# Optimization experiments

Hardware: AMD Instinct MI355X
Metric: run time of the kernel (lower is better)

The kernel has to match this reference:

```python
import jax, jax.numpy as jnp
import numpy as np

N, E, DN, DE, H, L = 2048, 32768, 512, 512, 8, 2
BN_EPS = 1e-5  # torch BatchNorm1d eps; eval mode with running_mean=0, running_var=1


def setup_inputs():
    key = jax.random.key(0)
    ks = jax.random.split(key, 12)
    rng = np.random.default_rng(0)
    # unique directed edges: 3E/4 upper-triangular pairs + reverses of the first E/4
    iu, ju = np.triu_indices(N, k=1)
    sel = rng.choice(iu.size, size=3 * E // 4, replace=False)
    s, d = iu[sel], ju[sel]
    src = np.concatenate([s, d[: E // 4]])
    dst = np.concatenate([d, s[: E // 4]])
    edge_index = jnp.asarray(np.stack([src, dst]).astype(np.int32))

    def p(k, shape, fan_in):
        return jax.random.normal(k, shape, jnp.float32) / np.sqrt(fan_in).astype(np.float32)

    return dict(
        x=jax.random.normal(ks[0], (N, DN), jnp.float32),
        edge_feature=jax.random.normal(ks[1], (E, DE), jnp.float32),
        node_pos=jax.random.uniform(ks[2], (N, 3), jnp.float32) * 10.0,
        inw=p(ks[3], (L, 3 * DN, DN), DN),          # MHA in_proj_weight per layer
        inb=jnp.zeros((L, 3 * DN), jnp.float32),
        ow=p(ks[4], (L, DN, DN), DN),               # MHA out_proj
        ob=jnp.zeros((L, DN), jnp.float32),
        etw=p(ks[5], (L, DE, DE), DE),              # edge_transform Linear
        etb=jnp.zeros((L, DE), jnp.float32),
        etg=jnp.ones((L, DE), jnp.float32),         # edge_transform BN gamma
        etbb=jnp.zeros((L, DE), jnp.float32),       # edge_transform BN beta
        unw=p(ks[6], (L, DN, DN + DE), DN + DE),    # update_node Linear
        unb=jnp.zeros((L, DN), jnp.float32),
        uew=p(ks[7], (L, DE, 2 * DN + 2 * DE), 2 * DN + 2 * DE),  # update_edge Linear
        ueb=jnp.zeros((L, DE), jnp.float32),
        edge_index=edge_index,
    )


def _forward(x, edge_feature, node_pos, inw, inb, ow, ob, etw, etb, etg, etbb, unw, unb, uew, ueb, edge_index):
    src, dst = edge_index[0], edge_index[1]
    n, e = x.shape[0], src.shape[0]
    hd = DN // H
    # vectorized reverse-edge lookup (mirrors the torch edge_dict)
    keys = src * n + dst
    rkeys = dst * n + src
    order = jnp.argsort(keys)
    sk = keys[order]
    pos = jnp.clip(jnp.searchsorted(sk, rkeys), 0, e - 1)
    found = sk[pos] == rkeys
    rev_idx = order[pos]
    # distance-based attention mask: -inf everywhere, 1/(dist+eps) on (symmetric) edges, 1.0 on diagonal
    diff = node_pos[src] - node_pos[dst]
    w = 1.0 / (jnp.sqrt(jnp.sum(diff * diff, axis=-1)) + 1e-6)
    mask = jnp.full((n, n), -jnp.inf, x.dtype)
    mask = mask.at[src, dst].set(w).at[dst, src].set(w)
    diag = jnp.arange(n)
    mask = mask.at[diag, diag].set(1.0)
    bn_scale = np.float32(1.0 / np.sqrt(1.0 + BN_EPS))
    nf, ef = x, edge_feature
    for l in range(L):
        rev = jnp.where(found[:, None], ef[rev_idx], 0.0)
        # MHSA over all nodes as one sequence (batch=1), eval mode (dropout off)
        qkv = nf @ inw[l].T + inb[l]
        q, k, v = [t.reshape(n, H, hd) for t in jnp.split(qkv, 3, axis=-1)]
        scores = jnp.einsum('nhd,mhd->hnm', q * np.float32(1.0 / np.sqrt(hd)), k) + mask
        attn = jax.nn.softmax(scores, axis=-1)
        ctx = jnp.einsum('hnm,mhd->nhd', attn, v).reshape(n, DN)
        x_upd = ctx @ ow[l].T + ob[l]
        # message: update_edge on [x_i, e, e_rev, x_j] (flow=target_to_source -> x_i = x[src])
        upd_edge = jnp.concatenate([nf[src], ef, rev, nf[dst]], axis=1) @ uew[l].T + ueb[l]
        # edge_transform = Linear + BN(eval) + ReLU
        te = jax.nn.relu((ef @ etw[l].T + etb[l]) * bn_scale * etg[l] + etbb[l])
        # scatter-max to subject/object nodes (empty segments -> 0, torch_scatter convention)
        subj = jax.ops.segment_max(te, src, num_segments=n)
        obj = jax.ops.segment_max(te, dst, num_segments=n)
        subj = jnp.where(jnp.isneginf(subj), 0.0, subj)
        obj = jnp.where(jnp.isneginf(obj), 0.0, obj)
        nf = jnp.concatenate([x_upd, subj + obj], axis=1) @ unw[l].T + unb[l]
        ef = upd_edge
        if l < L - 1 or L == 1:
            nf = jax.nn.relu(nf)
            ef = jax.nn.relu(ef)
    return nf, ef


def reference(x, edge_feature, node_pos, inw, inb, ow, ob, etw, etb, etg, etbb, unw, unb, uew, ueb, edge_index):
    return _forward(x, edge_feature, node_pos, inw, inb, ow, ob, etw, etb, etg, etbb, unw, unb, uew, ueb, edge_index)
```

## Files before the change

### kernel.cpp

```cpp
#include <hip/hip_runtime.h>
#include <hip/hip_bf16.h>

#define NN 2048
#define EE 32768
#define DND 512
#define NH 8
#define HD 64
#define MAXD 128
#define NEGF (-1e30f)
#define BN_SCALE 0.9999950000374997f

typedef __attribute__((ext_vector_type(8))) short bf16x8;
typedef __attribute__((ext_vector_type(4))) float f32x4;
typedef unsigned short u16;
typedef unsigned int u32;

static __device__ __forceinline__ float4 ld4(const float* p) {
    return *reinterpret_cast<const float4*>(p);
}
static __device__ __forceinline__ u16 f2b(float f) {
    __hip_bfloat16 h = __float2bfloat16(f);
    return *reinterpret_cast<u16*>(&h);
}
static __device__ __forceinline__ float b2f(u32 bits) {
    return __uint_as_float(bits << 16);
}
static __device__ __forceinline__ void gl_lds(const u16* g, u16* l) {
    __builtin_amdgcn_global_load_lds((const __attribute__((address_space(1))) void*)g,
                                     (__attribute__((address_space(3))) void*)l, 16, 0, 0);
}


__global__ __launch_bounds__(256) void init_table_k(int* __restrict__ t) {
    int i = blockIdx.x * 256 + threadIdx.x;
    t[i] = -1;
}

__global__ __launch_bounds__(256) void fill_table_k(const int* __restrict__ ei, int* __restrict__ t) {
    int e = blockIdx.x * 256 + threadIdx.x;
    if (e < EE) t[(size_t)ei[e] * NN + ei[EE + e]] = e;
}

__global__ __launch_bounds__(256) void build_rev_k(const int* __restrict__ ei, const int* __restrict__ t,
                                                   int* __restrict__ rev) {
    int e = blockIdx.x * 256 + threadIdx.x;
    if (e < EE) rev[e] = t[(size_t)ei[EE + e] * NN + ei[e]];
}

__global__ __launch_bounds__(256) void init_csr_k(int* __restrict__ adj, float* __restrict__ wadj,
                                                  int* __restrict__ cnt) {
    int i = blockIdx.x * 256 + threadIdx.x;
    if (i < NN) { cnt[i] = 1; adj[i * MAXD] = i; wadj[i * MAXD] = 1.0f; }
}

__global__ __launch_bounds__(256) void fill_csr_k(const int* __restrict__ ei, const int* __restrict__ rev,
                                                  const float* __restrict__ pos,
                                                  int* __restrict__ adj, float* __restrict__ wadj,
                                                  int* __restrict__ cnt) {
    int e = blockIdx.x * 256 + threadIdx.x;
    if (e >= EE) return;
    int s = ei[e], d = ei[EE + e];
    float dx = pos[s * 3 + 0] - pos[d * 3 + 0];
    float dy = pos[s * 3 + 1] - pos[d * 3 + 1];
    float dz = pos[s * 3 + 2] - pos[d * 3 + 2];
    float w = 1.0f / (sqrtf(dx * dx + dy * dy + dz * dz) + 1e-6f);
    int slot = atomicAdd(&cnt[s], 1);
    if (slot < MAXD) { adj[s * MAXD + slot] = d; wadj[s * MAXD + slot] = w; }
    if (rev[e] < 0) {
        slot = atomicAdd(&cnt[d], 1);
        if (slot < MAXD) { adj[d * MAXD + slot] = s; wadj[d * MAXD + slot] = w; }
    }
}

__global__ __launch_bounds__(256) void init_ecsr_k(int* __restrict__ ocnt, int* __restrict__ icnt) {
    int i = blockIdx.x * 256 + threadIdx.x;
    if (i < NN) { ocnt[i] = 0; icnt[i] = 0; }
}

__global__ __launch_bounds__(256) void fill_ecsr_k(const int* __restrict__ ei,
                                                   int* __restrict__ oadj, int* __restrict__ ocnt,
                                                   int* __restrict__ iadj, int* __restrict__ icnt) {
    int e = blockIdx.x * 256 + threadIdx.x;
    if (e >= EE) return;
    int s = ei[e], d = ei[EE + e];
    int slot = atomicAdd(&ocnt[s], 1);
    if (slot < MAXD) oadj[s * MAXD + slot] = e;
    slot = atomicAdd(&icnt[d], 1);
    if (slot < MAXD) iadj[d * MAXD + slot] = e;
}

__global__ __launch_bounds__(256) void conv_k(const float* __restrict__ src, u16* __restrict__ dst) {
    int i = (blockIdx.x * 256 + threadIdx.x) * 8;
    float4 a = ld4(src + i), b = ld4(src + i + 4);
    u16 o[8];
    o[0] = f2b(a.x); o[1] = f2b(a.y); o[2] = f2b(a.z); o[3] = f2b(a.w);
    o[4] = f2b(b.x); o[5] = f2b(b.y); o[6] = f2b(b.z); o[7] = f2b(b.w);
    *reinterpret_cast<int4*>(dst + i) = *reinterpret_cast<const int4*>(o);
}

__global__ __launch_bounds__(256) void gather_max_k(const u16* __restrict__ te,
                                                    const int* __restrict__ oadj, const int* __restrict__ ocnt,
                                                    const int* __restrict__ iadj, const int* __restrict__ icnt,
                                                    u16* __restrict__ sums)
{
    const int i = blockIdx.x;
    const int c2 = threadIdx.x;
    float ms0 = 0.f, ms1 = 0.f, mo0 = 0.f, mo1 = 0.f;
    int no = ocnt[i]; if (no > MAXD) no = MAXD;
    for (int s = 0; s < no; ++s) {
        const int e = oadj[i * MAXD + s];
        const u32 v = *reinterpret_cast<const u32*>(te + (size_t)e * DND + c2 * 2);
        ms0 = fmaxf(ms0, b2f(v & 0xffffu));
        ms1 = fmaxf(ms1, b2f(v >> 16));
    }
    int ni = icnt[i]; if (ni > MAXD) ni = MAXD;
    for (int s = 0; s < ni; ++s) {
        const int e = iadj[i * MAXD + s];
        const u32 v = *reinterpret_cast<const u32*>(te + (size_t)e * DND + c2 * 2);
        mo0 = fmaxf(mo0, b2f(v & 0xffffu));
        mo1 = fmaxf(mo1, b2f(v >> 16));
    }
    const u32 r = (u32)f2b(ms0 + mo0) | ((u32)f2b(ms1 + mo1) << 16);
    *reinterpret_cast<u32*>(sums + (size_t)i * DND + c2 * 2) = r;
}

template <int MODE, int EPI, int WF32, int WBF16, int GY>
__global__ __launch_bounds__(256) void mgemm_k(
    const u16* __restrict__ WS, u32 a_off, u32 b_off, const float* __restrict__ bias,
    float* __restrict__ Cf, u16* __restrict__ Cb, int M, int Nc, int K,
    u32 g0_off, u32 g1_off, u32 gz_off,
    const int* __restrict__ srcv, const int* __restrict__ dstv, const int* __restrict__ revv,
    const float* __restrict__ eg, const float* __restrict__ eb)
{
    __shared__ u16 As2[2][8192];
    __shared__ u16 Bs2[2][8192];
    const int tid = threadIdx.x, lane = tid & 63, w = tid >> 6;
    const int wr = w >> 1, wc = w & 1;
    const int b = blockIdx.x;
    const int xcd = b & 7, kb = b >> 3;
    const int bm = ((kb / GY) * 8 + xcd) * 128;
    const int bn = (kb % GY) * 128;

    const int rl = lane >> 3;
    const u32 lx = (u32)(((lane & 7) ^ rl) * 8);

    u32 offA0[4], offA1[4], offA2[4], offA3[4], offB[4];
#pragma unroll
    for (int q = 0; q < 4; ++q) {
        const int ra = bm + w * 32 + q * 8 + rl;
        if (MODE == 0) {
            offA0[q] = a_off + (u32)ra * (u32)K + lx;
        } else if (MODE == 1) {
            offA0[q] = g0_off + (u32)srcv[ra] * 512u + lx;
            offA1[q] = g1_off + (u32)ra * 512u + lx;
            const int rv = revv[ra];
            offA2[q] = (rv >= 0 ? g1_off + (u32)rv * 512u : gz_off) + lx;
            offA3[q] = g0_off + (u32)dstv[ra] * 512u + lx;
        } else {
            offA0[q] = g0_off + (u32)ra * 512u + lx;
            offA1[q] = g1_off + (u32)ra * 512u + lx;
        }
        offB[q] = b_off + (u32)(bn + w * 32 + q * 8 + rl) * (u32)K + lx;
    }

    const int nks = K >> 6;
    const int kq = lane >> 4, li = lane & 15;

    auto stage = [&](int t, int buf) {
        const u32 k0 = (u32)t * 64u;
        const int seg = (MODE == 0) ? 0 : (int)(k0 >> 9);
#pragma unroll
        for (int q = 0; q < 4; ++q) {
            u32 oa;
            if (MODE == 0)      oa = offA0[q];
            else if (MODE == 1) oa = (seg == 0 ? offA0[q] : seg == 1 ? offA1[q] : seg == 2 ? offA2[q] : offA3[q]);
            else                oa = (seg == 0 ? offA0[q] : offA1[q]);
            const u32 koff = (MODE == 0) ? k0 : (k0 & 511u);
            gl_lds(WS + oa + koff, &As2[buf][(w * 32 + q * 8) * 64]);
        }
#pragma unroll
        for (int q = 0; q < 4; ++q)
            gl_lds(WS + offB[q] + k0, &Bs2[buf][(w * 32 + q * 8) * 64]);
    };

    f32x4 acc[4][4] = {};
    const int baseA = (wr * 64 + li) * 64 + ((kq ^ (li & 7)) * 8);
    const int baseB = (wc * 64 + li) * 64 + ((kq ^ (li & 7)) * 8);

    stage(0, 0);
    for (int t = 0; t < nks; ++t) {
        const int cur = t & 1;
        if (t + 1 < nks) stage(t + 1, cur ^ 1);
        if (t + 1 < nks) asm volatile("s_waitcnt vmcnt(8)" ::: "memory");
        else             asm volatile("s_waitcnt vmcnt(0)" ::: "memory");
        __builtin_amdgcn_s_barrier();
        __builtin_amdgcn_sched_barrier(0);
#pragma unroll
        for (int sub = 0; sub < 2; ++sub) {
            const int sx = sub << 5;
            bf16x8 af[4], bf[4];
#pragma unroll
            for (int m = 0; m < 4; ++m)
                af[m] = *reinterpret_cast<const bf16x8*>(&As2[cur][(baseA + m * 1024) ^ sx]);
#pragma unroll
            for (int n = 0; n < 4; ++n)
                bf[n] = *reinterpret_cast<const bf16x8*>(&Bs2[cur][(baseB + n * 1024) ^ sx]);
#pragma unroll
            for (int m = 0; m < 4; ++m)
#pragma unroll
                for (int n = 0; n < 4; ++n)
                    acc[m][n] = __builtin_amdgcn_mfma_f32_16x16x32_bf16(af[m], bf[n], acc[m][n], 0, 0, 0);
        }
        __builtin_amdgcn_s_barrier();
        __builtin_amdgcn_sched_barrier(0);
    }

    float bsv[4], scv[4], shv[4];
#pragma unroll
    for (int n = 0; n < 4; ++n) {
        const int col = bn + wc * 64 + n * 16 + li;
        bsv[n] = bias[col];
        if (EPI == 2) { scv[n] = BN_SCALE * eg[col]; shv[n] = eb[col]; }
    }
#pragma unroll
    for (int m = 0; m < 4; ++m) {
#pragma unroll
        for (int n = 0; n < 4; ++n) {
            const int col = bn + wc * 64 + n * 16 + li;
#pragma unroll
            for (int i = 0; i < 4; ++i) {
                float v = acc[m][n][i] + bsv[n];
                if (EPI == 2) v = fmaxf(fmaf(v, scv[n], shv[n]), 0.f);
                else if (EPI == 1) v = fmaxf(v, 0.f);
                const int r = bm + wr * 64 + m * 16 + (lane >> 4) * 4 + i;
                if (WF32) Cf[(size_t)r * Nc + col] = v;
                if (WBF16) Cb[(size_t)r * Nc + col] = f2b(v);
            }
        }
    }
}

__global__ __launch_bounds__(256) void attn_sp_k(const float* __restrict__ qkv,
                                                 const int* __restrict__ adj,
                                                 const float* __restrict__ wadj,
                                                 const int* __restrict__ cnt,
                                                 u16* __restrict__ ctxb)
{
    const int i = blockIdx.x;
    const int wv = threadIdx.x >> 6, lane = threadIdx.x & 63;
    const int h = blockIdx.y * 4 + wv;
    __shared__ float qs[4][64];
    qs[wv][lane] = qkv[(size_t)i * 1536 + h * HD + lane] * 0.125f;
    __syncthreads();
    int deg = cnt[i];
    if (deg > MAXD) deg = MAXD;
    float m = -3.0e38f, lsum = 0.f, c = 0.f;
    for (int base = 0; base < deg; base += 64) {
        int nn_ = deg - base; if (nn_ > 64) nn_ = 64;
        int j = 0;
        float s = NEGF;
        if (lane < nn_) {
            j = adj[i * MAXD + base + lane];
            const float wgt = wadj[i * MAXD + base + lane];
            const float* kr = qkv + (size_t)j * 1536 + DND + h * HD;
            float accd = 0.f;
#pragma unroll
            for (int d4 = 0; d4 < 16; ++d4) {
                float4 kv = ld4(kr + d4 * 4);
                accd = fmaf(qs[wv][d4 * 4 + 0], kv.x, accd);
                accd = fmaf(qs[wv][d4 * 4 + 1], kv.y, accd);
                accd = fmaf(qs[wv][d4 * 4 + 2], kv.z, accd);
                accd = fmaf(qs[wv][d4 * 4 + 3], kv.w, accd);
            }
            s = accd + wgt;
        }
        float mloc = s;
#pragma unroll
        for (int o = 1; o < 64; o <<= 1) mloc = fmaxf(mloc, __shfl_xor(mloc, o, 64));
        const float mnew = fmaxf(m, mloc);
        const float alpha = __expf(m - mnew);
        const float p = (lane < nn_) ? __expf(s - mnew) : 0.f;
        float ps = p;
#pragma unroll
        for (int o = 1; o < 64; o <<= 1) ps += __shfl_xor(ps, o, 64);
        lsum = lsum * alpha + ps;
        c *= alpha;
        for (int l = 0; l < nn_; ++l) {
            const float pj = __shfl(p, l, 64);
            const int jj = __shfl(j, l, 64);
            c = fmaf(pj, qkv[(size_t)jj * 1536 + 2 * DND + h * HD + lane], c);
        }
        m = mnew;
    }
    ctxb[(size_t)i * DND + h * HD + lane] = f2b(c / lsum);
}

extern "C" void kernel_launch(void* const* d_in, const int* in_sizes, int n_in,
                              void* d_out, int out_size, void* d_ws, size_t ws_size,
                              hipStream_t stream)
{
    const float* x    = (const float*)d_in[0];
    const float* efin = (const float*)d_in[1];
    const float* pos  = (const float*)d_in[2];
    const float* inw  = (const float*)d_in[3];
    const float* inb  = (const float*)d_in[4];
    const float* ow   = (const float*)d_in[5];
    const float* ob   = (const float*)d_in[6];
    const float* etw  = (const float*)d_in[7];
    const float* etb  = (const float*)d_in[8];
    const float* etg  = (const float*)d_in[9];
    const float* etbb = (const float*)d_in[10];
    const float* unw  = (const float*)d_in[11];
    const float* unb  = (const float*)d_in[12];
    const float* uew  = (const float*)d_in[13];
    const float* ueb  = (const float*)d_in[14];
    const int*   ei   = (const int*)d_in[15];

    float* W = (float*)d_ws;
    float* qkv   = W;
    u16*   te    = (u16*)W;
    int*   rev   = (int*)(W + 8388608);
    u16*   zero  = (u16*)(W + 8421376);
    int*   adj   = (int*)(W + 8421888);
    float* wadj  = W + 8684032;
    int*   cnt   = (int*)(W + 8946176);
    int*   oadj  = (int*)(W + 8948224);
    int*   ocnt  = (int*)(W + 9210368);
    int*   iadj  = (int*)(W + 9212416);
    int*   icnt  = (int*)(W + 9474560);
    u16*   ctxb  = (u16*)(W + 9476608);
    u16*   xupdb = (u16*)(W + 10000896);
    u16*   sums  = (u16*)(W + 10525184);
    u16*   nfb   = (u16*)(W + 11049472);
    u16*   wbf   = (u16*)(W + 11573760);
    u16*   efbA  = (u16*)(W + 14457344);
    u16*   efbB  = (u16*)(W + 22845952);
    int*   table = (int*)efbA;

    u16* inwb = wbf;
    u16* owb  = wbf + 1572864;
    u16* etwb = wbf + 2097152;
    u16* unwb = wbf + 2621440;
    u16* uewb = wbf + 3670016;

    float* out_nf = (float*)d_out;
    float* out_ef = out_nf + (size_t)NN * DND;

    const int* srcv = ei;
    const int* dstv = ei + EE;

    const u16* WSu = (const u16*)d_ws;
    auto uoff = [&](const void* p) { return (u32)((const u16*)p - WSu); };

    init_table_k<<<NN * NN / 256, 256, 0, stream>>>(table);
    fill_table_k<<<EE / 256, 256, 0, stream>>>(ei, table);
    build_rev_k<<<EE / 256, 256, 0, stream>>>(ei, table, rev);
    init_csr_k<<<NN / 256, 256, 0, stream>>>(adj, wadj, cnt);
    fill_csr_k<<<EE / 256, 256, 0, stream>>>(ei, rev, pos, adj, wadj, cnt);
    init_ecsr_k<<<NN / 256, 256, 0, stream>>>(ocnt, icnt);
    fill_ecsr_k<<<EE / 256, 256, 0, stream>>>(ei, oadj, ocnt, iadj, icnt);
    hipMemsetAsync(zero, 0, 2048, stream);

    conv_k<<<1572864 / 2048, 256, 0, stream>>>(inw, inwb);
    conv_k<<<524288 / 2048, 256, 0, stream>>>(ow, owb);
    conv_k<<<524288 / 2048, 256, 0, stream>>>(etw, etwb);
    conv_k<<<1048576 / 2048, 256, 0, stream>>>(unw, unwb);
    conv_k<<<2097152 / 2048, 256, 0, stream>>>(uew, uewb);
    conv_k<<<1048576 / 2048, 256, 0, stream>>>(x, nfb);
    conv_k<<<16777216 / 2048, 256, 0, stream>>>(efin, efbA);

    for (int l = 0; l < 2; ++l) {
        const u16* efb_cur = l ? efbB : efbA;
        const u16* inwb_l = inwb + (size_t)l * 786432;
        const u16* owb_l  = owb  + (size_t)l * 262144;
        const u16* etwb_l = etwb + (size_t)l * 262144;
        const u16* unwb_l = unwb + (size_t)l * 524288;
        const u16* uewb_l = uewb + (size_t)l * 1048576;
        const float* inb_l  = inb  + (size_t)l * 1536;
        const float* ob_l   = ob   + (size_t)l * 512;
        const float* etb_l  = etb  + (size_t)l * 512;
        const float* etg_l  = etg  + (size_t)l * 512;
        const float* etbb_l = etbb + (size_t)l * 512;
        const float* unb_l  = unb  + (size_t)l * 512;
        const float* ueb_l  = ueb  + (size_t)l * 512;

        mgemm_k<0, 0, 1, 0, 12><<<192, 256, 0, stream>>>(
            WSu, uoff(nfb), uoff(inwb_l), inb_l, qkv, nullptr, NN, 3 * DND, DND,
            0, 0, 0, nullptr, nullptr, nullptr, nullptr, nullptr);

        attn_sp_k<<<dim3(NN, 2), 256, 0, stream>>>(qkv, adj, wadj, cnt, ctxb);

        mgemm_k<0, 0, 0, 1, 4><<<64, 256, 0, stream>>>(
            WSu, uoff(ctxb), uoff(owb_l), ob_l, nullptr, xupdb, NN, DND, DND,
            0, 0, 0, nullptr, nullptr, nullptr, nullptr, nullptr);

        mgemm_k<0, 2, 0, 1, 4><<<1024, 256, 0, stream>>>(
            WSu, uoff(efb_cur), uoff(etwb_l), etb_l, nullptr, te, EE, DND, DND,
            0, 0, 0, nullptr, nullptr, nullptr, etg_l, etbb_l);

        gather_max_k<<<NN, 256, 0, stream>>>(te, oadj, ocnt, iadj, icnt, sums);

        if (l == 0)
            mgemm_k<1, 1, 0, 1, 4><<<1024, 256, 0, stream>>>(
                WSu, 0, uoff(uewb_l), ueb_l, nullptr, efbB, EE, DND, 2048,
                uoff(nfb), uoff(efb_cur), uoff(zero), srcv, dstv, rev, nullptr, nullptr);
        else
            mgemm_k<1, 0, 1, 0, 4><<<1024, 256, 0, stream>>>(
                WSu, 0, uoff(uewb_l), ueb_l, out_ef, nullptr, EE, DND, 2048,
                uoff(nfb), uoff(efb_cur), uoff(zero), srcv, dstv, rev, nullptr, nullptr);

        if (l == 0)
            mgemm_k<2, 1, 0, 1, 4><<<64, 256, 0, stream>>>(
                WSu, 0, uoff(unwb_l), unb_l, nullptr, nfb, NN, DND, 1024,
                uoff(xupdb), uoff(sums), 0, nullptr, nullptr, nullptr, nullptr, nullptr);
        else
            mgemm_k<2, 0, 1, 0, 4><<<64, 256, 0, stream>>>(
                WSu, 0, uoff(unwb_l), unb_l, out_nf, nullptr, NN, DND, 1024,
                uoff(xupdb), uoff(sums), 0, nullptr, nullptr, nullptr, nullptr, nullptr);
    }
}
```

Measured before the change: 509.9 us.

## Factor update_edge GEMM into per-node projections plus per-edge partial GEMMs

Splits the update_edge weight into four column blocks. The node blocks (src and dst) are applied once per node in a 2048x1024 GEMM. The reverse-edge block is applied once per edge in a separate GEMM, and the self-edge block is applied in the main edge GEMM, whose epilogue gathers and adds the node projections and the reverse-edge projection. This replaces the K=2048 gathered GEMM over E edges with two K=512 edge GEMMs plus a small node GEMM, removing the redundant per-edge recomputation of node projections. In exchange it adds a bf16 intermediate round trip for the partial results, which costs some precision, and random gathers in the epilogue.

```diff
diff --git a/kernel.cpp b/kernel.cpp
--- a/kernel.cpp
+++ b/kernel.cpp
@@ -98,6 +98,18 @@
     *reinterpret_cast<int4*>(dst + i) = *reinterpret_cast<const int4*>(o);
 }
 
+__global__ __launch_bounds__(256) void convs_k(const float* __restrict__ src, u16* __restrict__ dst,
+                                               int stride, int c0) {
+    int idx = blockIdx.x * 256 + threadIdx.x;
+    int r = idx >> 6, c = (idx & 63) * 8;
+    const float* s = src + (size_t)r * stride + c0 + c;
+    float4 a = ld4(s), b = ld4(s + 4);
+    u16 o[8];
+    o[0] = f2b(a.x); o[1] = f2b(a.y); o[2] = f2b(a.z); o[3] = f2b(a.w);
+    o[4] = f2b(b.x); o[5] = f2b(b.y); o[6] = f2b(b.z); o[7] = f2b(b.w);
+    *reinterpret_cast<int4*>(dst + r * 512 + c) = *reinterpret_cast<const int4*>(o);
+}
+
 __global__ __launch_bounds__(256) void gather_max_k(const u16* __restrict__ te,
                                                     const int* __restrict__ oadj, const int* __restrict__ ocnt,
                                                     const int* __restrict__ iadj, const int* __restrict__ icnt,
@@ -128,9 +140,10 @@
 __global__ __launch_bounds__(256) void mgemm_k(
     const u16* __restrict__ WS, u32 a_off, u32 b_off, const float* __restrict__ bias,
     float* __restrict__ Cf, u16* __restrict__ Cb, int M, int Nc, int K,
-    u32 g0_off, u32 g1_off, u32 gz_off,
+    u32 g0_off, u32 g1_off,
     const int* __restrict__ srcv, const int* __restrict__ dstv, const int* __restrict__ revv,
-    const float* __restrict__ eg, const float* __restrict__ eb)
+    const float* __restrict__ eg, const float* __restrict__ eb,
+    const u16* __restrict__ Pb, const u16* __restrict__ Q2b)
 {
     __shared__ u16 As2[2][8192];
     __shared__ u16 Bs2[2][8192];
@@ -144,18 +157,12 @@
     const int rl = lane >> 3;
     const u32 lx = (u32)(((lane & 7) ^ rl) * 8);
 
-    u32 offA0[4], offA1[4], offA2[4], offA3[4], offB[4];
+    u32 offA0[4], offA1[4], offB[4];
 #pragma unroll
     for (int q = 0; q < 4; ++q) {
         const int ra = bm + w * 32 + q * 8 + rl;
         if (MODE == 0) {
             offA0[q] = a_off + (u32)ra * (u32)K + lx;
-        } else if (MODE == 1) {
-            offA0[q] = g0_off + (u32)srcv[ra] * 512u + lx;
-            offA1[q] = g1_off + (u32)ra * 512u + lx;
-            const int rv = revv[ra];
-            offA2[q] = (rv >= 0 ? g1_off + (u32)rv * 512u : gz_off) + lx;
-            offA3[q] = g0_off + (u32)dstv[ra] * 512u + lx;
         } else {
             offA0[q] = g0_off + (u32)ra * 512u + lx;
             offA1[q] = g1_off + (u32)ra * 512u + lx;
@@ -172,9 +179,8 @@
 #pragma unroll
         for (int q = 0; q < 4; ++q) {
             u32 oa;
-            if (MODE == 0)      oa = offA0[q];
-            else if (MODE == 1) oa = (seg == 0 ? offA0[q] : seg == 1 ? offA1[q] : seg == 2 ? offA2[q] : offA3[q]);
-            else                oa = (seg == 0 ? offA0[q] : offA1[q]);
+            if (MODE == 0) oa = offA0[q];
+            else           oa = (seg == 0 ? offA0[q] : offA1[q]);
             const u32 koff = (MODE == 0) ? k0 : (k0 & 511u);
             gl_lds(WS + oa + koff, &As2[buf][(w * 32 + q * 8) * 64]);
         }
@@ -224,14 +230,30 @@
     }
 #pragma unroll
     for (int m = 0; m < 4; ++m) {
+        int sr[4], dr[4], rv[4];
+        if (EPI == 3 || EPI == 4) {
+#pragma unroll
+            for (int i = 0; i < 4; ++i) {
+                const int r = bm + wr * 64 + m * 16 + (lane >> 4) * 4 + i;
+                sr[i] = srcv[r]; dr[i] = dstv[r]; rv[i] = revv[r];
+            }
+        }
 #pragma unroll
         for (int n = 0; n < 4; ++n) {
             const int col = bn + wc * 64 + n * 16 + li;
 #pragma unroll
             for (int i = 0; i < 4; ++i) {
                 float v = acc[m][n][i] + bsv[n];
-                if (EPI == 2) v = fmaxf(fmaf(v, scv[n], shv[n]), 0.f);
-                else if (EPI == 1) v = fmaxf(v, 0.f);
+                if (EPI == 2) {
+                    v = fmaxf(fmaf(v, scv[n], shv[n]), 0.f);
+                } else if (EPI == 1) {
+                    v = fmaxf(v, 0.f);
+                } else if (EPI == 3 || EPI == 4) {
+                    v += b2f((u32)Pb[(size_t)sr[i] * 1024 + col]);
+                    v += b2f((u32)Pb[(size_t)dr[i] * 1024 + 512 + col]);
+                    if (rv[i] >= 0) v += b2f((u32)Q2b[(size_t)rv[i] * 512 + col]);
+                    if (EPI == 3) v = fmaxf(v, 0.f);
+                }
                 const int r = bm + wr * 64 + m * 16 + (lane >> 4) * 4 + i;
                 if (WF32) Cf[(size_t)r * Nc + col] = v;
                 if (WBF16) Cb[(size_t)r * Nc + col] = f2b(v);
@@ -318,30 +340,32 @@
 
     float* W = (float*)d_ws;
     float* qkv   = W;
-    u16*   te    = (u16*)W;
+    u16*   unib  = (u16*)W;
     int*   rev   = (int*)(W + 8388608);
-    u16*   zero  = (u16*)(W + 8421376);
-    int*   adj   = (int*)(W + 8421888);
-    float* wadj  = W + 8684032;
-    int*   cnt   = (int*)(W + 8946176);
-    int*   oadj  = (int*)(W + 8948224);
-    int*   ocnt  = (int*)(W + 9210368);
-    int*   iadj  = (int*)(W + 9212416);
-    int*   icnt  = (int*)(W + 9474560);
-    u16*   ctxb  = (u16*)(W + 9476608);
-    u16*   xupdb = (u16*)(W + 10000896);
-    u16*   sums  = (u16*)(W + 10525184);
-    u16*   nfb   = (u16*)(W + 11049472);
-    u16*   wbf   = (u16*)(W + 11573760);
-    u16*   efbA  = (u16*)(W + 14457344);
-    u16*   efbB  = (u16*)(W + 22845952);
+    float* zeroz = W + 8421376;
+    int*   adj   = (int*)(W + 8423424);
+    float* wadj  = W + 8685568;
+    int*   cnt   = (int*)(W + 8947712);
+    int*   oadj  = (int*)(W + 8949760);
+    int*   ocnt  = (int*)(W + 9211904);
+    int*   iadj  = (int*)(W + 9213952);
+    int*   icnt  = (int*)(W + 9476096);
+    u16*   ctxb  = (u16*)(W + 9478144);
+    u16*   xupdb = (u16*)(W + 10002432);
+    u16*   sums  = (u16*)(W + 10526720);
+    u16*   nfb   = (u16*)(W + 11051008);
+    u16*   wbf   = (u16*)(W + 11575296);
+    u16*   efbA  = (u16*)(W + 14458880);
+    u16*   efbB  = (u16*)(W + 22847488);
     int*   table = (int*)efbA;
 
     u16* inwb = wbf;
     u16* owb  = wbf + 1572864;
     u16* etwb = wbf + 2097152;
     u16* unwb = wbf + 2621440;
-    u16* uewb = wbf + 3670016;
+    u16* w1b  = wbf + 3670016;
+    u16* w2b  = wbf + 4194304;
+    u16* pwb  = wbf + 4718592;
 
     float* out_nf = (float*)d_out;
     float* out_ef = out_nf + (size_t)NN * DND;
@@ -359,23 +383,33 @@
     fill_csr_k<<<EE / 256, 256, 0, stream>>>(ei, rev, pos, adj, wadj, cnt);
     init_ecsr_k<<<NN / 256, 256, 0, stream>>>(ocnt, icnt);
     fill_ecsr_k<<<EE / 256, 256, 0, stream>>>(ei, oadj, ocnt, iadj, icnt);
-    hipMemsetAsync(zero, 0, 2048, stream);
+    hipMemsetAsync(zeroz, 0, 8192, stream);
 
     conv_k<<<1572864 / 2048, 256, 0, stream>>>(inw, inwb);
     conv_k<<<524288 / 2048, 256, 0, stream>>>(ow, owb);
     conv_k<<<524288 / 2048, 256, 0, stream>>>(etw, etwb);
     conv_k<<<1048576 / 2048, 256, 0, stream>>>(unw, unwb);
-    conv_k<<<2097152 / 2048, 256, 0, stream>>>(uew, uewb);
+    for (int l = 0; l < 2; ++l) {
+        const float* uew_l = uew + (size_t)l * DND * 2048;
+        convs_k<<<128, 256, 0, stream>>>(uew_l, w1b + l * 262144, 2048, 512);
+        convs_k<<<128, 256, 0, stream>>>(uew_l, w2b + l * 262144, 2048, 1024);
+        convs_k<<<128, 256, 0, stream>>>(uew_l, pwb + l * 524288, 2048, 0);
+        convs_k<<<128, 256, 0, stream>>>(uew_l, pwb + l * 524288 + 262144, 2048, 1536);
+    }
     conv_k<<<1048576 / 2048, 256, 0, stream>>>(x, nfb);
     conv_k<<<16777216 / 2048, 256, 0, stream>>>(efin, efbA);
 
     for (int l = 0; l < 2; ++l) {
         const u16* efb_cur = l ? efbB : efbA;
+        u16* Pb = l ? efbA : (u16*)out_ef;
+        u16* Q2b = unib;
         const u16* inwb_l = inwb + (size_t)l * 786432;
         const u16* owb_l  = owb  + (size_t)l * 262144;
         const u16* etwb_l = etwb + (size_t)l * 262144;
         const u16* unwb_l = unwb + (size_t)l * 524288;
-        const u16* uewb_l = uewb + (size_t)l * 1048576;
+        const u16* w1b_l  = w1b  + (size_t)l * 262144;
+        const u16* w2b_l  = w2b  + (size_t)l * 262144;
+        const u16* pwb_l  = pwb  + (size_t)l * 524288;
         const float* inb_l  = inb  + (size_t)l * 1536;
         const float* ob_l   = ob   + (size_t)l * 512;
         const float* etb_l  = etb  + (size_t)l * 512;
@@ -385,37 +419,45 @@
         const float* ueb_l  = ueb  + (size_t)l * 512;
 
         mgemm_k<0, 0, 1, 0, 12><<<192, 256, 0, stream>>>(
-            WSu, uoff(nfb), uoff(inwb_l), inb_l, qkv, nullptr, NN, 3 * DND, DND,
-            0, 0, 0, nullptr, nullptr, nullptr, nullptr, nullptr);
+            WSu, uoff(nfb), uoff(inwb_l), inb_l, qkv, nullptr, NN, 1536, DND,
+            0, 0, nullptr, nullptr, nullptr, nullptr, nullptr, nullptr, nullptr);
 
         attn_sp_k<<<dim3(NN, 2), 256, 0, stream>>>(qkv, adj, wadj, cnt, ctxb);
 
         mgemm_k<0, 0, 0, 1, 4><<<64, 256, 0, stream>>>(
             WSu, uoff(ctxb), uoff(owb_l), ob_l, nullptr, xupdb, NN, DND, DND,
-            0, 0, 0, nullptr, nullptr, nullptr, nullptr, nullptr);
+            0, 0, nullptr, nullptr, nullptr, nullptr, nullptr, nullptr, nullptr);
+
+        mgemm_k<0, 0, 0, 1, 8><<<128, 256, 0, stream>>>(
+            WSu, uoff(nfb), uoff(pwb_l), zeroz, nullptr, Pb, NN, 1024, DND,
+            0, 0, nullptr, nullptr, nullptr, nullptr, nullptr, nullptr, nullptr);
+
+        mgemm_k<0, 0, 0, 1, 4><<<1024, 256, 0, stream>>>(
+            WSu, uoff(efb_cur), uoff(w2b_l), zeroz, nullptr, Q2b, EE, DND, DND,
+            0, 0, nullptr, nullptr, nullptr, nullptr, nullptr, nullptr, nullptr);
+
+        if (l == 0)
+            mgemm_k<0, 3, 0, 1, 4><<<1024, 256, 0, stream>>>(
+                WSu, uoff(efb_cur), uoff(w1b_l), ueb_l, nullptr, efbB, EE, DND, DND,
+                0, 0, srcv, dstv, rev, nullptr, nullptr, Pb, Q2b);
+        else
+            mgemm_k<0, 4, 1, 0, 4><<<1024, 256, 0, stream>>>(
+                WSu, uoff(efb_cur), uoff(w1b_l), ueb_l, out_ef, nullptr, EE, DND, DND,
+                0, 0, srcv, dstv, rev, nullptr, nullptr, Pb, Q2b);
 
         mgemm_k<0, 2, 0, 1, 4><<<1024, 256, 0, stream>>>(
-            WSu, uoff(efb_cur), uoff(etwb_l), etb_l, nullptr, te, EE, DND, DND,
-            0, 0, 0, nullptr, nullptr, nullptr, etg_l, etbb_l);
-
-        gather_max_k<<<NN, 256, 0, stream>>>(te, oadj, ocnt, iadj, icnt, sums);
-
-        if (l == 0)
-            mgemm_k<1, 1, 0, 1, 4><<<1024, 256, 0, stream>>>(
-                WSu, 0, uoff(uewb_l), ueb_l, nullptr, efbB, EE, DND, 2048,
-                uoff(nfb), uoff(efb_cur), uoff(zero), srcv, dstv, rev, nullptr, nullptr);
-        else
-            mgemm_k<1, 0, 1, 0, 4><<<1024, 256, 0, stream>>>(
-                WSu, 0, uoff(uewb_l), ueb_l, out_ef, nullptr, EE, DND, 2048,
-                uoff(nfb), uoff(efb_cur), uoff(zero), srcv, dstv, rev, nullptr, nullptr);
+            WSu, uoff(efb_cur), uoff(etwb_l), etb_l, nullptr, unib, EE, DND, DND,
+            0, 0, nullptr, nullptr, nullptr, etg_l, etbb_l, nullptr, nullptr);
+
+        gather_max_k<<<NN, 256, 0, stream>>>(unib, oadj, ocnt, iadj, icnt, sums);
 
         if (l == 0)
             mgemm_k<2, 1, 0, 1, 4><<<64, 256, 0, stream>>>(
                 WSu, 0, uoff(unwb_l), unb_l, nullptr, nfb, NN, DND, 1024,
-                uoff(xupdb), uoff(sums), 0, nullptr, nullptr, nullptr, nullptr, nullptr);
+                uoff(xupdb), uoff(sums), nullptr, nullptr, nullptr, nullptr, nullptr, nullptr, nullptr);
         else
             mgemm_k<2, 0, 1, 0, 4><<<64, 256, 0, stream>>>(
                 WSu, 0, uoff(unwb_l), unb_l, out_nf, nullptr, NN, DND, 1024,
-                uoff(xupdb), uoff(sums), 0, nullptr, nullptr, nullptr, nullptr, nullptr);
-    }
-}
+                uoff(xupdb), uoff(sums), nullptr, nullptr, nullptr, nullptr, nullptr, nullptr, nullptr);
+    }
+}
```

Result: slower. 558.9 us (+9.6%).

## Use 256x256 block tiles with 512 threads for edge-sized GEMMs

Applied to the files above, without the earlier changes.

Adds a new GEMM kernel with 256x256 output tiles, 8 waves and a single 128KB shared buffer (double-buffered A and B). It replaces the 128x128 kernel for the edge_transform and update_edge GEMMs over the 32768 edges. The gather-concatenated MODE 1 path moves from the old kernel into the new one. Larger tiles halve global reloads of A and B per FLOP, in exchange for more registers (8x4 accumulators), higher LDS use, and fewer blocks (256), which lowers occupancy and the number of waves for latency hiding.

```diff
diff --git a/kernel.cpp b/kernel.cpp
--- a/kernel.cpp
+++ b/kernel.cpp
@@ -144,18 +144,12 @@
     const int rl = lane >> 3;
     const u32 lx = (u32)(((lane & 7) ^ rl) * 8);
 
-    u32 offA0[4], offA1[4], offA2[4], offA3[4], offB[4];
+    u32 offA0[4], offA1[4], offB[4];
 #pragma unroll
     for (int q = 0; q < 4; ++q) {
         const int ra = bm + w * 32 + q * 8 + rl;
         if (MODE == 0) {
             offA0[q] = a_off + (u32)ra * (u32)K + lx;
-        } else if (MODE == 1) {
-            offA0[q] = g0_off + (u32)srcv[ra] * 512u + lx;
-            offA1[q] = g1_off + (u32)ra * 512u + lx;
-            const int rv = revv[ra];
-            offA2[q] = (rv >= 0 ? g1_off + (u32)rv * 512u : gz_off) + lx;
-            offA3[q] = g0_off + (u32)dstv[ra] * 512u + lx;
         } else {
             offA0[q] = g0_off + (u32)ra * 512u + lx;
             offA1[q] = g1_off + (u32)ra * 512u + lx;
@@ -171,10 +165,7 @@
         const int seg = (MODE == 0) ? 0 : (int)(k0 >> 9);
 #pragma unroll
         for (int q = 0; q < 4; ++q) {
-            u32 oa;
-            if (MODE == 0)      oa = offA0[q];
-            else if (MODE == 1) oa = (seg == 0 ? offA0[q] : seg == 1 ? offA1[q] : seg == 2 ? offA2[q] : offA3[q]);
-            else                oa = (seg == 0 ? offA0[q] : offA1[q]);
+            u32 oa = (MODE == 0) ? offA0[q] : (seg == 0 ? offA0[q] : offA1[q]);
             const u32 koff = (MODE == 0) ? k0 : (k0 & 511u);
             gl_lds(WS + oa + koff, &As2[buf][(w * 32 + q * 8) * 64]);
         }
@@ -233,6 +224,116 @@
                 if (EPI == 2) v = fmaxf(fmaf(v, scv[n], shv[n]), 0.f);
                 else if (EPI == 1) v = fmaxf(v, 0.f);
                 const int r = bm + wr * 64 + m * 16 + (lane >> 4) * 4 + i;
+                if (WF32) Cf[(size_t)r * Nc + col] = v;
+                if (WBF16) Cb[(size_t)r * Nc + col] = f2b(v);
+            }
+        }
+    }
+}
+
+template <int MODE, int EPI, int WF32, int WBF16>
+__global__ __launch_bounds__(512, 2) void mgemm256_k(
+    const u16* __restrict__ WS, u32 a_off, u32 b_off, const float* __restrict__ bias,
+    float* __restrict__ Cf, u16* __restrict__ Cb, int M, int Nc, int K,
+    u32 g0_off, u32 g1_off, u32 gz_off,
+    const int* __restrict__ srcv, const int* __restrict__ dstv, const int* __restrict__ revv,
+    const float* __restrict__ eg, const float* __restrict__ eb)
+{
+    __shared__ u16 SB[65536];
+    const int tid = threadIdx.x, lane = tid & 63, w = tid >> 6;
+    const int wr = w >> 2, wc = w & 3;
+    const int b = blockIdx.x;
+    const int bm = ((b & 7) + 8 * (b >> 4)) * 256;
+    const int bn = ((b >> 3) & 1) * 256;
+
+    const int rl = lane >> 3;
+    const u32 lx = (u32)(((lane & 7) ^ rl) * 8);
+
+    u32 offA0[4], offA1[4], offA2[4], offA3[4], offB[4];
+#pragma unroll
+    for (int q = 0; q < 4; ++q) {
+        const int ra = bm + w * 32 + q * 8 + rl;
+        if (MODE == 0) {
+            offA0[q] = a_off + (u32)ra * (u32)K + lx;
+        } else {
+            offA0[q] = g0_off + (u32)srcv[ra] * 512u + lx;
+            offA1[q] = g1_off + (u32)ra * 512u + lx;
+            const int rv = revv[ra];
+            offA2[q] = (rv >= 0 ? g1_off + (u32)rv * 512u : gz_off) + lx;
+            offA3[q] = g0_off + (u32)dstv[ra] * 512u + lx;
+        }
+        offB[q] = b_off + (u32)(bn + w * 32 + q * 8 + rl) * (u32)K + lx;
+    }
+
+    const int nks = K >> 6;
+    const int kq = lane >> 4, li = lane & 15;
+
+    auto stage = [&](int t, int buf) {
+        const u32 k0 = (u32)t * 64u;
+        const int seg = (MODE == 0) ? 0 : (int)(k0 >> 9);
+#pragma unroll
+        for (int q = 0; q < 4; ++q) {
+            u32 oa;
+            if (MODE == 0) oa = offA0[q];
+            else           oa = (seg == 0 ? offA0[q] : seg == 1 ? offA1[q] : seg == 2 ? offA2[q] : offA3[q]);
+            const u32 koff = (MODE == 0) ? k0 : (k0 & 511u);
+            gl_lds(WS + oa + koff, &SB[buf * 16384 + (w * 32 + q * 8) * 64]);
+        }
+#pragma unroll
+        for (int q = 0; q < 4; ++q)
+            gl_lds(WS + offB[q] + k0, &SB[32768 + buf * 16384 + (w * 32 + q * 8) * 64]);
+    };
+
+    f32x4 acc[8][4] = {};
+    const int baseA = (wr * 128 + li) * 64 + ((kq ^ (li & 7)) * 8);
+    const int baseB = (wc * 64 + li) * 64 + ((kq ^ (li & 7)) * 8);
+
+    stage(0, 0);
+    for (int t = 0; t < nks; ++t) {
+        const int cur = t & 1;
+        if (t + 1 < nks) stage(t + 1, cur ^ 1);
+        if (t + 1 < nks) asm volatile("s_waitcnt vmcnt(8)" ::: "memory");
+        else             asm volatile("s_waitcnt vmcnt(0)" ::: "memory");
+        __builtin_amdgcn_s_barrier();
+        __builtin_amdgcn_sched_barrier(0);
+#pragma unroll
+        for (int sub = 0; sub < 2; ++sub) {
+            const int sx = sub << 5;
+            bf16x8 af[8], bf[4];
+#pragma unroll
+            for (int m = 0; m < 8; ++m)
+                af[m] = *reinterpret_cast<const bf16x8*>(&SB[(cur * 16384 + baseA + m * 1024) ^ sx]);
+#pragma unroll
+            for (int n = 0; n < 4; ++n)
+                bf[n] = *reinterpret_cast<const bf16x8*>(&SB[(32768 + cur * 16384 + baseB + n * 1024) ^ sx]);
+#pragma unroll
+            for (int m = 0; m < 8; ++m)
+#pragma unroll
+                for (int n = 0; n < 4; ++n)
+                    acc[m][n] = __builtin_amdgcn_mfma_f32_16x16x32_bf16(af[m], bf[n], acc[m][n], 0, 0, 0);
+        }
+        __builtin_amdgcn_s_barrier();
+        __builtin_amdgcn_sched_barrier(0);
+    }
+
+    float bsv[4], scv[4], shv[4];
+#pragma unroll
+    for (int n = 0; n < 4; ++n) {
+        const int col = bn + wc * 64 + n * 16 + li;
+        bsv[n] = bias[col];
+        if (EPI == 2) { scv[n] = BN_SCALE * eg[col]; shv[n] = eb[col]; }
+    }
+#pragma unroll
+    for (int m = 0; m < 8; ++m) {
+#pragma unroll
+        for (int n = 0; n < 4; ++n) {
+            const int col = bn + wc * 64 + n * 16 + li;
+#pragma unroll
+            for (int i = 0; i < 4; ++i) {
+                float v = acc[m][n][i] + bsv[n];
+                if (EPI == 2) v = fmaxf(fmaf(v, scv[n], shv[n]), 0.f);
+                else if (EPI == 1) v = fmaxf(v, 0.f);
+                const int r = bm + wr * 128 + m * 16 + (lane >> 4) * 4 + i;
                 if (WF32) Cf[(size_t)r * Nc + col] = v;
                 if (WBF16) Cb[(size_t)r * Nc + col] = f2b(v);
             }
@@ -385,7 +486,7 @@
         const float* ueb_l  = ueb  + (size_t)l * 512;
 
         mgemm_k<0, 0, 1, 0, 12><<<192, 256, 0, stream>>>(
-            WSu, uoff(nfb), uoff(inwb_l), inb_l, qkv, nullptr, NN, 3 * DND, DND,
+            WSu, uoff(nfb), uoff(inwb_l), inb_l, qkv, nullptr, NN, 1536, DND,
             0, 0, 0, nullptr, nullptr, nullptr, nullptr, nullptr);
 
         attn_sp_k<<<dim3(NN, 2), 256, 0, stream>>>(qkv, adj, wadj, cnt, ctxb);
@@ -394,18 +495,18 @@
             WSu, uoff(ctxb), uoff(owb_l), ob_l, nullptr, xupdb, NN, DND, DND,
             0, 0, 0, nullptr, nullptr, nullptr, nullptr, nullptr);
 
-        mgemm_k<0, 2, 0, 1, 4><<<1024, 256, 0, stream>>>(
+        mgemm256_k<0, 2, 0, 1><<<256, 512, 0, stream>>>(
             WSu, uoff(efb_cur), uoff(etwb_l), etb_l, nullptr, te, EE, DND, DND,
             0, 0, 0, nullptr, nullptr, nullptr, etg_l, etbb_l);
 
         gather_max_k<<<NN, 256, 0, stream>>>(te, oadj, ocnt, iadj, icnt, sums);
 
         if (l == 0)
-            mgemm_k<1, 1, 0, 1, 4><<<1024, 256, 0, stream>>>(
+            mgemm256_k<1, 1, 0, 1><<<256, 512, 0, stream>>>(
                 WSu, 0, uoff(uewb_l), ueb_l, nullptr, efbB, EE, DND, 2048,
                 uoff(nfb), uoff(efb_cur), uoff(zero), srcv, dstv, rev, nullptr, nullptr);
         else
-            mgemm_k<1, 0, 1, 0, 4><<<1024, 256, 0, stream>>>(
+            mgemm256_k<1, 0, 1, 0><<<256, 512, 0, stream>>>(
                 WSu, 0, uoff(uewb_l), ueb_l, out_ef, nullptr, EE, DND, 2048,
                 uoff(nfb), uoff(efb_cur), uoff(zero), srcv, dstv, rev, nullptr, nullptr);
 
```

Measured after the change: 468.5 us. 8.1% less time.
